# Optimization experiments

Hardware: AMD Instinct MI355X
Metric: run time of the kernel (lower is better)

Reference implementation:

```python
import jax, jax.numpy as jnp
import numpy as np

E, B, C = 4, 262144, 128  # edge types, tokens, feature dim

def setup_inputs() -> dict:
    key = jax.random.key(0)
    k1, k2, k3 = jax.random.split(key, 3)
    xs = jax.random.normal(k1, (E, B, C), dtype=jnp.float32)
    Ws = jax.random.normal(k2, (E, C, C), dtype=jnp.float32) * (1.0 / np.sqrt(C))
    bs = jax.random.normal(k3, (E, C), dtype=jnp.float32) * 0.01
    return {"xs": xs, "Ws": Ws, "bs": bs}

def reference(xs, Ws, bs):
    # Per-edge-type op: y_e = xs[e] @ Ws[e] + bs[e]  (Linear per from_node type)
    # Aggregation: sum over edges.
    # Fused grouped form: contract over edge axis e and input channel c in one einsum.
    out = jnp.einsum('ebc,ecd->bd', xs, Ws)          # [B, C]
    out = out + bs.sum(axis=0)                       # bias from each edge op, summed by aggregation
    return out
```

## Files before the change

### kernel.cpp

```cpp
#include <hip/hip_runtime.h>
#include <hip/hip_bf16.h>

#define N_E 4
#define N_B 262144
#define N_C 128

typedef __attribute__((ext_vector_type(8))) short bf16x8;
typedef __attribute__((ext_vector_type(4))) float f32x4;
typedef __attribute__((ext_vector_type(4))) unsigned int u32x4;

__device__ __forceinline__ unsigned pk2(float lo, float hi) {
  float2 t; t.x = lo; t.y = hi;
  __hip_bfloat162 h = __float22bfloat162_rn(t);
  union { __hip_bfloat162 h; unsigned u; } c;
  c.h = h;
  return c.u;
}

__global__ void __launch_bounds__(1024, 4)
grouped_gemm(const float* __restrict__ xs, const float* __restrict__ Ws,
             const float* __restrict__ bs, float* __restrict__ out) {
  extern __shared__ unsigned char smem[];
  unsigned short* lds_w = (unsigned short*)smem;

  const int tid  = threadIdx.x;
  const int lane = tid & 63;
  const int wave = tid >> 6;
  const int l15  = lane & 15;
  const int hi   = lane >> 4;
  const int waveRow = blockIdx.x * 256 + wave * 16;

  float bias[8];
#pragma unroll
  for (int n = 0; n < 8; ++n) {
    int d = n * 16 + l15;
    bias[n] = bs[d] + bs[128 + d] + bs[256 + d] + bs[384 + d];
  }

#pragma unroll
  for (int i = 0; i < 8; ++i) {
    int m = tid + i * 1024;
    int e = m >> 11;
    int g = (m >> 7) & 15;
    int d = m & 127;
    int kt = g >> 2, h2 = g & 3;
    const float* src = Ws + e * (N_C * N_C) + (kt * 32 + h2 * 4) * N_C + d;
    float v[8];
#pragma unroll
    for (int j = 0; j < 4; ++j) v[j] = src[j * N_C];
#pragma unroll
    for (int j = 0; j < 4; ++j) v[4 + j] = src[(16 + j) * N_C];
    u32x4 pk;
#pragma unroll
    for (int j = 0; j < 4; ++j) pk[j] = pk2(v[2 * j], v[2 * j + 1]);
    *reinterpret_cast<u32x4*>(&lds_w[(size_t)m * 8]) = pk;
  }

  asm volatile("s_waitcnt vmcnt(0)" ::: "memory");
  __syncthreads();

  const unsigned vb = (unsigned)(waveRow + l15) * 512u + (unsigned)hi * 16u;
  const unsigned long long xbase = (unsigned long long)xs;

  f32x4 A0[4], A1[4];

#define AISSUE(c)                                                              \
  do {                                                                         \
    unsigned o;                                                                \
    asm volatile("v_add_u32 %0, %1, %2"                                        \
                 : "=v"(o)                                                     \
                 : "n"(((c) >> 2) * 134217728u + ((c) & 3) * 128u), "v"(vb));  \
    asm volatile("global_load_dwordx4 %0, %2, %3 offset:0\n\t"                 \
                 "global_load_dwordx4 %1, %2, %3 offset:64"                    \
                 : "=&v"(A0[(c) & 3]), "=&v"(A1[(c) & 3])                      \
                 : "v"(o), "s"(xbase)                                          \
                 : "memory");                                                  \
  } while (0)

#define WAITV(n)                                          \
  do {                                                    \
    asm volatile("s_waitcnt vmcnt(" #n ")" ::: "memory"); \
    __builtin_amdgcn_sched_barrier(0);                    \
  } while (0)

  f32x4 acc[8];
#pragma unroll
  for (int n = 0; n < 8; ++n) {
    f32x4 z = {0.0f, 0.0f, 0.0f, 0.0f};
    acc[n] = z;
  }

  AISSUE(0); AISSUE(1); AISSUE(2); AISSUE(3);

#define STEP(s, w)                                                             \
  do {                                                                         \
    WAITV(w);                                                                  \
    f32x4 a0 = A0[(s) & 3];                                                    \
    f32x4 a1 = A1[(s) & 3];                                                    \
    bf16x8 afrag;                                                              \
    unsigned* au = reinterpret_cast<unsigned*>(&afrag);                        \
    au[0] = pk2(a0[0], a0[1]);                                                 \
    au[1] = pk2(a0[2], a0[3]);                                                 \
    au[2] = pk2(a1[0], a1[1]);                                                 \
    au[3] = pk2(a1[2], a1[3]);                                                 \
    if ((s) <= 11) AISSUE((s) + 4);                                            \
    const unsigned short* wb =                                                 \
        lds_w + (size_t)((((s) >> 2) * 16 + ((s) & 3) * 4 + hi) * 128 + l15) * 8; \
    _Pragma("unroll")                                                          \
    for (int n = 0; n < 8; ++n) {                                              \
      bf16x8 bfrag = *reinterpret_cast<const bf16x8*>(wb + (size_t)n * 128);   \
      acc[n] = __builtin_amdgcn_mfma_f32_16x16x32_bf16(afrag, bfrag, acc[n], 0, 0, 0); \
    }                                                                          \
  } while (0)

  STEP(0, 6);  STEP(1, 6);  STEP(2, 6);  STEP(3, 6);
  STEP(4, 6);  STEP(5, 6);  STEP(6, 6);  STEP(7, 6);
  STEP(8, 6);  STEP(9, 6);  STEP(10, 6); STEP(11, 6);
  STEP(12, 6); STEP(13, 4); STEP(14, 2); STEP(15, 0);

#undef STEP
#undef WAITV
#undef AISSUE

#pragma unroll
  for (int n = 0; n < 8; ++n) {
    int d = n * 16 + l15;
#pragma unroll
    for (int r = 0; r < 4; ++r) {
      int row = waveRow + hi * 4 + r;
      out[(size_t)row * N_C + d] = acc[n][r] + bias[n];
    }
  }
}

extern "C" void kernel_launch(void* const* d_in, const int* in_sizes, int n_in,
                              void* d_out, int out_size, void* d_ws, size_t ws_size,
                              hipStream_t stream) {
  const float* xs = (const float*)d_in[0];
  const float* Ws = (const float*)d_in[1];
  const float* bs = (const float*)d_in[2];
  float* out = (float*)d_out;

  const size_t smem = 131072;
  hipFuncSetAttribute((const void*)grouped_gemm,
                      hipFuncAttributeMaxDynamicSharedMemorySize, (int)smem);

  dim3 grid(N_B / 256);
  dim3 block(1024);
  hipLaunchKernelGGL(grouped_gemm, grid, block, smem, stream, xs, Ws, bs, out);
}
```

Measured before the change: 146.2 us.

## Switch to 32x32x16 bf16 MFMA with 512-thread blocks and deeper prefetch

Replaces the 16x16x32 MFMA tiling with 32x32x16 MFMA. Each wave now covers 32 rows, and the block shrinks to 8 waves of 512 threads. The LDS weight layout, the A-fragment load offsets and the output row mapping are reworked to match. The global-load prefetch ring is deepened from 4 to 6 stages over 32 k-steps. The aim is fewer LDS B-fragment reads per FLOP and better latency hiding on this memory-bound kernel. The cost is higher accumulator register pressure and half as many threads to load the shared weights.

Measured after the change: 146.9 us. Within noise of the previous version (+0.4%).

```diff
diff --git a/kernel.cpp b/kernel.cpp
--- a/kernel.cpp
+++ b/kernel.cpp
@@ -7,6 +7,7 @@
 
 typedef __attribute__((ext_vector_type(8))) short bf16x8;
 typedef __attribute__((ext_vector_type(4))) float f32x4;
+typedef __attribute__((ext_vector_type(16))) float f32x16;
 typedef __attribute__((ext_vector_type(4))) unsigned int u32x4;
 
 __device__ __forceinline__ unsigned pk2(float lo, float hi) {
@@ -17,7 +18,7 @@
   return c.u;
 }
 
-__global__ void __launch_bounds__(1024, 4)
+__global__ void __launch_bounds__(512, 2)
 grouped_gemm(const float* __restrict__ xs, const float* __restrict__ Ws,
              const float* __restrict__ bs, float* __restrict__ out) {
   extern __shared__ unsigned char smem[];
@@ -26,30 +27,29 @@
   const int tid  = threadIdx.x;
   const int lane = tid & 63;
   const int wave = tid >> 6;
-  const int l15  = lane & 15;
-  const int hi   = lane >> 4;
-  const int waveRow = blockIdx.x * 256 + wave * 16;
+  const int col5 = lane & 31;
+  const int h    = lane >> 5;
+  const int waveRow = blockIdx.x * 256 + wave * 32;
 
-  float bias[8];
+  float bias[4];
 #pragma unroll
-  for (int n = 0; n < 8; ++n) {
-    int d = n * 16 + l15;
+  for (int n = 0; n < 4; ++n) {
+    int d = n * 32 + col5;
     bias[n] = bs[d] + bs[128 + d] + bs[256 + d] + bs[384 + d];
   }
 
 #pragma unroll
-  for (int i = 0; i < 8; ++i) {
-    int m = tid + i * 1024;
-    int e = m >> 11;
-    int g = (m >> 7) & 15;
-    int d = m & 127;
-    int kt = g >> 2, h2 = g & 3;
-    const float* src = Ws + e * (N_C * N_C) + (kt * 32 + h2 * 4) * N_C + d;
+  for (int i = 0; i < 16; ++i) {
+    int m = tid + i * 512;
+    int e  = m >> 11;
+    int kt = (m >> 8) & 7;
+    int n  = (m >> 6) & 3;
+    int h2 = (m >> 5) & 1;
+    int c5 = m & 31;
+    const float* src = Ws + e * (N_C * N_C) + (kt * 16 + h2 * 8) * N_C + n * 32 + c5;
     float v[8];
 #pragma unroll
-    for (int j = 0; j < 4; ++j) v[j] = src[j * N_C];
-#pragma unroll
-    for (int j = 0; j < 4; ++j) v[4 + j] = src[(16 + j) * N_C];
+    for (int j = 0; j < 8; ++j) v[j] = src[j * N_C];
     u32x4 pk;
 #pragma unroll
     for (int j = 0; j < 4; ++j) pk[j] = pk2(v[2 * j], v[2 * j + 1]);
@@ -59,20 +59,20 @@
   asm volatile("s_waitcnt vmcnt(0)" ::: "memory");
   __syncthreads();
 
-  const unsigned vb = (unsigned)(waveRow + l15) * 512u + (unsigned)hi * 16u;
+  const unsigned vb = (unsigned)(waveRow + col5) * 512u + (unsigned)h * 32u;
   const unsigned long long xbase = (unsigned long long)xs;
 
-  f32x4 A0[4], A1[4];
+  f32x4 A0[6], A1[6];
 
-#define AISSUE(c)                                                              \
+#define AISSUE(s)                                                              \
   do {                                                                         \
     unsigned o;                                                                \
     asm volatile("v_add_u32 %0, %1, %2"                                        \
                  : "=v"(o)                                                     \
-                 : "n"(((c) >> 2) * 134217728u + ((c) & 3) * 128u), "v"(vb));  \
+                 : "n"((((s) >> 3) * 134217728u) + (((s) & 7) * 64u)), "v"(vb)); \
     asm volatile("global_load_dwordx4 %0, %2, %3 offset:0\n\t"                 \
-                 "global_load_dwordx4 %1, %2, %3 offset:64"                    \
-                 : "=&v"(A0[(c) & 3]), "=&v"(A1[(c) & 3])                      \
+                 "global_load_dwordx4 %1, %2, %3 offset:16"                    \
+                 : "=&v"(A0[(s) % 6]), "=&v"(A1[(s) % 6])                      \
                  : "v"(o), "s"(xbase)                                          \
                  : "memory");                                                  \
   } while (0)
@@ -83,51 +83,55 @@
     __builtin_amdgcn_sched_barrier(0);                    \
   } while (0)
 
-  f32x4 acc[8];
+  f32x16 acc[4];
 #pragma unroll
-  for (int n = 0; n < 8; ++n) {
-    f32x4 z = {0.0f, 0.0f, 0.0f, 0.0f};
-    acc[n] = z;
+  for (int n = 0; n < 4; ++n) {
+#pragma unroll
+    for (int r = 0; r < 16; ++r) acc[n][r] = 0.0f;
   }
-
-  AISSUE(0); AISSUE(1); AISSUE(2); AISSUE(3);
 
 #define STEP(s, w)                                                             \
   do {                                                                         \
     WAITV(w);                                                                  \
-    f32x4 a0 = A0[(s) & 3];                                                    \
-    f32x4 a1 = A1[(s) & 3];                                                    \
+    f32x4 a0 = A0[(s) % 6];                                                    \
+    f32x4 a1 = A1[(s) % 6];                                                    \
     bf16x8 afrag;                                                              \
     unsigned* au = reinterpret_cast<unsigned*>(&afrag);                        \
     au[0] = pk2(a0[0], a0[1]);                                                 \
     au[1] = pk2(a0[2], a0[3]);                                                 \
     au[2] = pk2(a1[0], a1[1]);                                                 \
     au[3] = pk2(a1[2], a1[3]);                                                 \
-    if ((s) <= 11) AISSUE((s) + 4);                                            \
+    if ((s) <= 25) AISSUE((s) + 6);                                            \
     const unsigned short* wb =                                                 \
-        lds_w + (size_t)((((s) >> 2) * 16 + ((s) & 3) * 4 + hi) * 128 + l15) * 8; \
+        lds_w + ((size_t)((((s) >> 3) * 8 + ((s) & 7)) * 4) * 64 + lane) * 8;  \
     _Pragma("unroll")                                                          \
-    for (int n = 0; n < 8; ++n) {                                              \
-      bf16x8 bfrag = *reinterpret_cast<const bf16x8*>(wb + (size_t)n * 128);   \
-      acc[n] = __builtin_amdgcn_mfma_f32_16x16x32_bf16(afrag, bfrag, acc[n], 0, 0, 0); \
+    for (int n = 0; n < 4; ++n) {                                              \
+      bf16x8 bfrag = *reinterpret_cast<const bf16x8*>(wb + (size_t)n * 512);   \
+      acc[n] = __builtin_amdgcn_mfma_f32_32x32x16_bf16(afrag, bfrag, acc[n], 0, 0, 0); \
     }                                                                          \
   } while (0)
 
-  STEP(0, 6);  STEP(1, 6);  STEP(2, 6);  STEP(3, 6);
-  STEP(4, 6);  STEP(5, 6);  STEP(6, 6);  STEP(7, 6);
-  STEP(8, 6);  STEP(9, 6);  STEP(10, 6); STEP(11, 6);
-  STEP(12, 6); STEP(13, 4); STEP(14, 2); STEP(15, 0);
+  AISSUE(0); AISSUE(1); AISSUE(2); AISSUE(3); AISSUE(4); AISSUE(5);
+
+  STEP(0, 10);  STEP(1, 10);  STEP(2, 10);  STEP(3, 10);
+  STEP(4, 10);  STEP(5, 10);  STEP(6, 10);  STEP(7, 10);
+  STEP(8, 10);  STEP(9, 10);  STEP(10, 10); STEP(11, 10);
+  STEP(12, 10); STEP(13, 10); STEP(14, 10); STEP(15, 10);
+  STEP(16, 10); STEP(17, 10); STEP(18, 10); STEP(19, 10);
+  STEP(20, 10); STEP(21, 10); STEP(22, 10); STEP(23, 10);
+  STEP(24, 10); STEP(25, 10); STEP(26, 10);
+  STEP(27, 8);  STEP(28, 6);  STEP(29, 4);  STEP(30, 2);  STEP(31, 0);
 
 #undef STEP
 #undef WAITV
 #undef AISSUE
 
 #pragma unroll
-  for (int n = 0; n < 8; ++n) {
-    int d = n * 16 + l15;
+  for (int n = 0; n < 4; ++n) {
+    int d = n * 32 + col5;
 #pragma unroll
-    for (int r = 0; r < 4; ++r) {
-      int row = waveRow + hi * 4 + r;
+    for (int r = 0; r < 16; ++r) {
+      int row = waveRow + (r & 3) + 8 * (r >> 2) + 4 * h;
       out[(size_t)row * N_C + d] = acc[n][r] + bias[n];
     }
   }
@@ -146,6 +150,6 @@
                       hipFuncAttributeMaxDynamicSharedMemorySize, (int)smem);
 
   dim3 grid(N_B / 256);
-  dim3 block(1024);
+  dim3 block(512);
   hipLaunchKernelGGL(grouped_gemm, grid, block, smem, stream, xs, Ws, bs, out);
 }
```
